# Optimization experiments

Measured on AMD Instinct MI355X. Metric: run time of the kernel, lower is better.

The kernel has to match this reference:

```python
import jax, jax.numpy as jnp
import numpy as np

N_NODES = 100000
N_EDGES = 3200000
DIN, DHID, DOUT = 128, 128, 128


def setup_inputs() -> dict:
    key = jax.random.key(0)
    ks = jax.random.split(key, 8)
    x = jax.random.normal(ks[0], (N_NODES, DIN), dtype=jnp.float32)
    edge_index = jax.random.randint(ks[1], (2, N_EDGES), 0, N_NODES, dtype=jnp.int32)
    def glorot(k, fan_in, fan_out):
        s = jnp.sqrt(6.0 / (fan_in + fan_out)).astype(jnp.float32)
        return jax.random.uniform(k, (fan_in, fan_out), jnp.float32, -s, s)
    return {
        "x": x,
        "edge_index": edge_index,
        "w1": glorot(ks[2], DIN, DHID), "b1": jnp.zeros((DHID,), jnp.float32),
        "w2": glorot(ks[3], DHID, DHID), "b2": jnp.zeros((DHID,), jnp.float32),
        "w3": glorot(ks[4], DHID, DOUT), "b3": jnp.zeros((DOUT,), jnp.float32),
    }


def reference(x, edge_index, w1, b1, w2, b2, w3, b3):
    n = x.shape[0]
    # GCN normalization with self-loops (PyG gcn_norm, edge_weight = 1)
    loop = jnp.arange(n, dtype=edge_index.dtype)
    src = jnp.concatenate([edge_index[0], loop])  # [E+N]
    dst = jnp.concatenate([edge_index[1], loop])  # [E+N]
    deg = jax.ops.segment_sum(jnp.ones_like(dst, dtype=x.dtype), dst, num_segments=n)
    dinv = jnp.where(deg > 0, jax.lax.rsqrt(deg), 0.0)
    norm = dinv[src] * dinv[dst]  # [E+N]

    def gcn_conv(h, w, b):
        h = h @ w  # [N, dout]
        msg = norm[:, None] * h[src]  # gather + scale, [E+N, dout]
        agg = jax.ops.segment_sum(msg, dst, num_segments=n)  # scatter-add
        return agg + b

    h = jax.nn.relu(gcn_conv(x, w1, b1))
    h = jax.nn.relu(gcn_conv(h, w2, b2))  # dropout p=0 / eval: no-op
    h = gcn_conv(h, w3, b3)
    return jnp.sum(h, axis=0, keepdims=True) / h.shape[0]  # [1, DOUT]
```

## Files before the change

### kernel.cpp

```cpp
#include <hip/hip_runtime.h>

#define D 128
#define BSH 8
#define CAP 12288
#define CH 8192

typedef unsigned short ushort_t;
typedef unsigned int uint_t;
typedef unsigned char uchar_t;

typedef __attribute__((ext_vector_type(8))) short frag_ab;
typedef __attribute__((ext_vector_type(4))) float frag_cd;
typedef __attribute__((ext_vector_type(2))) float float2v;

union frag_u { ushort_t u[8]; frag_ab v; };


__device__ __forceinline__ float bf2f(ushort_t u) {
    union { uint_t i; float f; } v; v.i = ((uint_t)u) << 16; return v.f;
}
__device__ __forceinline__ ushort_t f2bf(float f) {
    union { float f; uint_t i; } v; v.f = f;
    uint_t u = v.i;
    u += 0x7fffu + ((u >> 16) & 1u);
    return (ushort_t)(u >> 16);
}

__device__ __forceinline__ void acc_fp8(uint_t w, float2v& aA, float2v& aB) {
    aA += __builtin_amdgcn_cvt_pk_f32_fp8(w, false);
    aB += __builtin_amdgcn_cvt_pk_f32_fp8(w, true);
}
__device__ __forceinline__ uint_t g8(const uint_t* __restrict__ t8, uint_t byteoff) {
    return *(const uint_t*)((const char*)t8 + byteoff);
}

__launch_bounds__(512)
__global__ void k_binpack(const int* __restrict__ src, const int* __restrict__ dst,
                          int* __restrict__ curA, int* __restrict__ curB,
                          uint_t* __restrict__ binA, uint_t* __restrict__ binB,
                          int E, int nb, int nbin,
                          const float* __restrict__ W1, const float* __restrict__ W2,
                          ushort_t* __restrict__ h1, ushort_t* __restrict__ l1,
                          ushort_t* __restrict__ h2, ushort_t* __restrict__ l2,
                          const float* __restrict__ b1, const float* __restrict__ b2,
                          float* __restrict__ bp1, float* __restrict__ bp2,
                          uint_t* __restrict__ zrow) {
    int tx = threadIdx.x;

    if (blockIdx.x >= nbin) {
        int wb = blockIdx.x - nbin;
        if (wb == 64) {
            if (tx < 128) {
                int c = (tx & 7) * 16 + (tx >> 3);
                bp1[tx] = b1[c];
                bp2[tx] = b2[c];
            }
            if (tx >= 128 && tx < 160) zrow[tx - 128] = 0;
            return;
        }
        int gid = wb * 512 + tx;
        int which = gid >> 14;
        int idx = gid & 16383;
        int k = idx >> 7, n = idx & 127;
        float w = which ? W2[(((k & 7) * 16) + (k >> 3)) * 128 + n] : W1[idx];
        ushort_t h = f2bf(w);
        ushort_t l = f2bf(w - bf2f(h));
        int c = k >> 5, quad = (k >> 3) & 3, jj = k & 7;
        int j = n >> 4, l16 = n & 15;
        int lane = quad * 16 + l16;
        int dest = ((c * 8 + j) * 64 + lane) * 8 + jj;
        if (which) { h2[dest] = h; l2[dest] = l; }
        else       { h1[dest] = h; l1[dest] = l; }
        return;
    }

    __shared__ int hA[512], hB[512], sc[512], gb[512];
    __shared__ ushort_t sbkt[CH];
    __shared__ uint_t sent[CH];
    hA[tx] = 0; hB[tx] = 0;
    __syncthreads();

    int e0 = blockIdx.x * CH;
    int e1 = min(e0 + CH, E);
    int total = e1 - e0;

    int sreg[16], dreg[16];
#pragma unroll
    for (int it = 0; it < 16; ++it) {
        int e = e0 + tx + it * 512;
        if (e < e1) {
            int s = src[e], d = dst[e];
            sreg[it] = s; dreg[it] = d;
            atomicAdd(&hA[d >> BSH], 1);
            atomicAdd(&hB[s >> BSH], 1);
        }
    }
    __syncthreads();

    {
        int v = hA[tx];
        sc[tx] = v;
        __syncthreads();
        for (int d = 1; d < 512; d <<= 1) {
            int t = (tx >= d) ? sc[tx - d] : 0;
            __syncthreads();
            sc[tx] += t;
            __syncthreads();
        }
        sc[tx] -= v;
        gb[tx] = v ? atomicAdd(&curA[tx], v) : 0;
        hA[tx] = 0;
        __syncthreads();
#pragma unroll
        for (int it = 0; it < 16; ++it) {
            int e = e0 + tx + it * 512;
            if (e < e1) {
                int s = sreg[it], d = dreg[it];
                int k = d >> BSH;
                int pos = sc[k] + atomicAdd(&hA[k], 1);
                sent[pos] = ((uint_t)s << 8) | (uint_t)(d & 255);
                sbkt[pos] = (ushort_t)k;
            }
        }
        __syncthreads();
        for (int p = tx; p < total; p += 512) {
            int k = sbkt[p];
            int gp = gb[k] + (p - sc[k]);
            if (gp < CAP) binA[(size_t)k * CAP + gp] = sent[p];
        }
        __syncthreads();
    }

    {
        int v = hB[tx];
        sc[tx] = v;
        __syncthreads();
        for (int d = 1; d < 512; d <<= 1) {
            int t = (tx >= d) ? sc[tx - d] : 0;
            __syncthreads();
            sc[tx] += t;
            __syncthreads();
        }
        sc[tx] -= v;
        gb[tx] = v ? atomicAdd(&curB[tx], v) : 0;
        hB[tx] = 0;
        __syncthreads();
#pragma unroll
        for (int it = 0; it < 16; ++it) {
            int e = e0 + tx + it * 512;
            if (e < e1) {
                int s = sreg[it], d = dreg[it];
                int k = s >> BSH;
                int pos = sc[k] + atomicAdd(&hB[k], 1);
                sent[pos] = ((uint_t)d << 8) | (uint_t)(s & 255);
                sbkt[pos] = (ushort_t)k;
            }
        }
        __syncthreads();
        for (int p = tx; p < total; p += 512) {
            int k = sbkt[p];
            int gp = gb[k] + (p - sc[k]);
            if (gp < CAP) binB[(size_t)k * CAP + gp] = sent[p];
        }
    }
}

__launch_bounds__(1024)
__global__ void k_csr(const uint_t* __restrict__ binA, const int* __restrict__ curA,
                      float* __restrict__ dinv, int* __restrict__ row_beg,
                      int* __restrict__ row_end, int* __restrict__ csr_src, int N) {
    __shared__ int hist[256];
    __shared__ int scan[256];
    __shared__ uint_t ebuf[CAP];
    int b = blockIdx.x;
    int tx = threadIdx.x;
    int cnt = min(curA[b], CAP);
    const uint_t* eb = binA + (size_t)b * CAP;

    if (tx < 256) hist[tx] = 0;
    __syncthreads();
    for (int e = tx; e < cnt; e += 1024) {
        uint_t pk = eb[e];
        ebuf[e] = pk;
        atomicAdd(&hist[pk & 255u], 1);
    }
    __syncthreads();
    int v = 0, pd = 0;
    if (tx < 256) {
        v = hist[tx];
        pd = (v + 15) & ~15;
        scan[tx] = pd;
    }
    __syncthreads();
    for (int dd = 1; dd < 256; dd <<= 1) {
        int t = 0;
        if (tx < 256 && tx >= dd) t = scan[tx - dd];
        __syncthreads();
        if (tx < 256) scan[tx] += t;
        __syncthreads();
    }
    if (tx < 256) {
        int my_excl = scan[tx] - pd;
        int node = b * 256 + tx;
        if (node < N) {
            dinv[node] = rsqrtf((float)(v + 1));
            row_beg[node] = b * CAP + my_excl;
            row_end[node] = b * CAP + my_excl + pd;
        }
        for (int i = v; i < pd; i++)
            csr_src[b * CAP + my_excl + i] = N;
        hist[tx] = my_excl;
    }
    __syncthreads();
    for (int e = tx; e < cnt; e += 1024) {
        uint_t pk = ebuf[e];
        int pos = b * CAP + atomicAdd(&hist[pk & 255u], 1);
        csr_src[pos] = (int)(pk >> 8);
    }
}

template <int IN_F32>
__launch_bounds__(256)
__global__ void gemm_mfma(const void* __restrict__ Av, const ushort_t* __restrict__ Whi,
                          const ushort_t* __restrict__ Wlo, const float* __restrict__ dinv,
                          uchar_t* __restrict__ C8, int nrows) {
    int wave = threadIdx.x >> 6;
    int lane = threadIdx.x & 63;
    int quad = lane >> 4, l16 = lane & 15;
    int base = blockIdx.x * 128 + wave * 32;

    frag_cd acc[2][8];
#pragma unroll
    for (int rt = 0; rt < 2; rt++)
#pragma unroll
        for (int j = 0; j < 8; j++) acc[rt][j] = (frag_cd)0.f;

    const ushort_t* Ab = (const ushort_t*)Av;
    const float* Af = (const float*)Av;

#pragma unroll
    for (int c = 0; c < 4; c++) {
        frag_ab afrag[2];
        int koff = c * 32 + quad * 8;
#pragma unroll
        for (int rt = 0; rt < 2; rt++) {
            int row = min(base + rt * 16 + l16, nrows - 1);
            if (IN_F32) {
                const float* ap = Af + (size_t)row * D + koff;
                float4 a0 = *(const float4*)ap;
                float4 a1 = *(const float4*)(ap + 4);
                frag_u fu;
                fu.u[0] = f2bf(a0.x); fu.u[1] = f2bf(a0.y);
                fu.u[2] = f2bf(a0.z); fu.u[3] = f2bf(a0.w);
                fu.u[4] = f2bf(a1.x); fu.u[5] = f2bf(a1.y);
                fu.u[6] = f2bf(a1.z); fu.u[7] = f2bf(a1.w);
                afrag[rt] = fu.v;
            } else {
                afrag[rt] = *(const frag_ab*)(Ab + (size_t)row * D + koff);
            }
        }
#pragma unroll
        for (int j = 0; j < 8; j++) {
            frag_ab bh = *(const frag_ab*)(Whi + (((c * 8 + j) * 64 + lane) * 8));
            frag_ab bl = *(const frag_ab*)(Wlo + (((c * 8 + j) * 64 + lane) * 8));
#pragma unroll
            for (int rt = 0; rt < 2; rt++) {
                acc[rt][j] = __builtin_amdgcn_mfma_f32_16x16x32_bf16(afrag[rt], bh,
                                                                     acc[rt][j], 0, 0, 0);
                acc[rt][j] = __builtin_amdgcn_mfma_f32_16x16x32_bf16(afrag[rt], bl,
                                                                     acc[rt][j], 0, 0, 0);
            }
        }
    }

#pragma unroll
    for (int rt = 0; rt < 2; rt++) {
        int rbase = base + rt * 16 + quad * 4;
#pragma unroll
        for (int reg = 0; reg < 4; reg++) {
            int row = rbase + reg;
            if (row < nrows) {
                float dv = dinv[row];
                uint_t d0 = (uint_t)__builtin_amdgcn_cvt_pk_fp8_f32(
                    acc[rt][0][reg] * dv, acc[rt][1][reg] * dv, 0, false);
                d0 = (uint_t)__builtin_amdgcn_cvt_pk_fp8_f32(
                    acc[rt][2][reg] * dv, acc[rt][3][reg] * dv, (int)d0, true);
                uint_t d1 = (uint_t)__builtin_amdgcn_cvt_pk_fp8_f32(
                    acc[rt][4][reg] * dv, acc[rt][5][reg] * dv, 0, false);
                d1 = (uint_t)__builtin_amdgcn_cvt_pk_fp8_f32(
                    acc[rt][6][reg] * dv, acc[rt][7][reg] * dv, (int)d1, true);
                uint2 o; o.x = d0; o.y = d1;
                *(uint2*)(C8 + (size_t)row * D + l16 * 8) = o;
            }
        }
    }
}

__launch_bounds__(256)
__global__ void agg8(const uint_t* __restrict__ t8, const int* __restrict__ csr_src,
                     const int* __restrict__ row_beg, const int* __restrict__ row_end,
                     const float* __restrict__ dinv, const float* __restrict__ bias,
                     uint_t* __restrict__ out, int n, int do_relu) {
    int node = blockIdx.x * 4 + (threadIdx.x >> 6);
    if (node >= n) return;
    int lane = threadIdx.x & 63;
    int eh = lane >> 5;
    uint_t cl = (uint_t)(lane & 31);
    uint_t cl4 = cl * 4u;

    int beg = row_beg[node];
    int cnt = row_end[node] - beg;
    float dn = dinv[node];

    float2v accA = {0.f, 0.f}, accB = {0.f, 0.f};

    if (eh == 0) {
        uint_t w = g8(t8, (uint_t)node * 128u + cl4);
        accA = __builtin_amdgcn_cvt_pk_f32_fp8(w, false);
        accB = __builtin_amdgcn_cvt_pk_f32_fp8(w, true);
    }

    int half = cnt >> 1;
    int e     = beg + (eh ? half : 0);
    int nfull = half >> 3;

    uint4 sa, sb;
    if (nfull > 0) {
        __builtin_memcpy(&sa, csr_src + e, 16);
        __builtin_memcpy(&sb, csr_src + e + 4, 16);
    }
    for (int it = 0; it < nfull; ++it) {
        uint4 ca = sa, cb = sb;
        e += 8;
        if (it + 1 < nfull) {
            __builtin_memcpy(&sa, csr_src + e, 16);
            __builtin_memcpy(&sb, csr_src + e + 4, 16);
        }
        uint_t w0 = g8(t8, ca.x * 128u + cl4);
        uint_t w1 = g8(t8, ca.y * 128u + cl4);
        uint_t w2 = g8(t8, ca.z * 128u + cl4);
        uint_t w3 = g8(t8, ca.w * 128u + cl4);
        uint_t w4 = g8(t8, cb.x * 128u + cl4);
        uint_t w5 = g8(t8, cb.y * 128u + cl4);
        uint_t w6 = g8(t8, cb.z * 128u + cl4);
        uint_t w7 = g8(t8, cb.w * 128u + cl4);
        acc_fp8(w0, accA, accB);
        acc_fp8(w1, accA, accB);
        acc_fp8(w2, accA, accB);
        acc_fp8(w3, accA, accB);
        acc_fp8(w4, accA, accB);
        acc_fp8(w5, accA, accB);
        acc_fp8(w6, accA, accB);
        acc_fp8(w7, accA, accB);
    }

    float a0 = accA.x, a1 = accA.y, a2 = accB.x, a3 = accB.y;
    a0 += __shfl(a0, lane ^ 32, 64);
    a1 += __shfl(a1, lane ^ 32, 64);
    a2 += __shfl(a2, lane ^ 32, 64);
    a3 += __shfl(a3, lane ^ 32, 64);

    if (eh == 0) {
        float4 bb = ((const float4*)bias)[cl];
        float o0 = dn * a0 + bb.x;
        float o1 = dn * a1 + bb.y;
        float o2 = dn * a2 + bb.z;
        float o3 = dn * a3 + bb.w;
        if (do_relu) {
            o0 = fmaxf(o0, 0.f); o1 = fmaxf(o1, 0.f);
            o2 = fmaxf(o2, 0.f); o3 = fmaxf(o3, 0.f);
        }
        uint2 ow;
        ow.x = (uint_t)f2bf(o0) | ((uint_t)f2bf(o1) << 16);
        ow.y = (uint_t)f2bf(o2) | ((uint_t)f2bf(o3) << 16);
        ((uint2*)out)[(size_t)node * 32 + cl] = ow;
    }
}

__launch_bounds__(512)
__global__ void wreduce_fin(const ushort_t* __restrict__ h, const uint_t* __restrict__ binB,
                            const int* __restrict__ curB, const float* __restrict__ dinv,
                            float* __restrict__ v, int n,
                            const float* __restrict__ w3, const float* __restrict__ b3,
                            float* __restrict__ out, float invn, int* __restrict__ done) {
    __shared__ float owacc[256];
    __shared__ float s[512];
    __shared__ int is_last;
    int b = blockIdx.x;
    int tx = threadIdx.x;
    if (tx < 256) owacc[tx] = 0.f;
    __syncthreads();
    int cnt = min(curB[b], CAP);
    const uint_t* eb = binB + (size_t)b * CAP;
    for (int e = tx; e < cnt; e += 512) {
        uint_t pk = eb[e];
        atomicAdd(&owacc[pk & 255u], dinv[pk >> 8]);
    }
    __syncthreads();

    int c = tx & 127;
    int rg = tx >> 7;
    int base = b * 256;
    int lim = min(base + 256, n);
    float acc = 0.f;
    for (int r = base + rg; r < lim; r += 4) {
        float dv = dinv[r];
        float cv = dv * (dv + owacc[r - base]);
        acc += cv * bf2f(h[(size_t)r * D + c]);
    }
    s[tx] = acc;
    __syncthreads();
    if (tx < 128)
        atomicAdd(&v[c], (s[tx] + s[tx + 128]) + (s[tx + 256] + s[tx + 384]));
    __syncthreads();

    if (tx == 0) {
        __threadfence();
        int old = atomicAdd(done, 1);
        is_last = (old == (int)gridDim.x - 1) ? 1 : 0;
    }
    __syncthreads();
    if (is_last) {
        __threadfence();
        if (tx < 128) owacc[tx] = ((volatile float*)v)[tx];
        __syncthreads();
        if (tx < 128) {
            float facc = 0.f;
            for (int k = 0; k < D; k++) {
                int p = (k & 15) * 8 + (k >> 4);
                facc += owacc[p] * w3[(size_t)k * D + tx];
            }
            out[tx] = facc * invn + b3[tx];
        }
    }
}

extern "C" void kernel_launch(void* const* d_in, const int* in_sizes, int n_in,
                              void* d_out, int out_size, void* d_ws, size_t ws_size,
                              hipStream_t stream) {
    const float* x   = (const float*)d_in[0];
    const int*   ei  = (const int*)d_in[1];
    const float* w1  = (const float*)d_in[2];
    const float* b1  = (const float*)d_in[3];
    const float* w2  = (const float*)d_in[4];
    const float* b2  = (const float*)d_in[5];
    const float* w3  = (const float*)d_in[6];
    const float* b3  = (const float*)d_in[7];
    float* out = (float*)d_out;

    const int N = in_sizes[0] / D;
    const int E = in_sizes[1] / 2;
    const int* src = ei;
    const int* dst = ei + E;
    const int nb = (N + 255) >> 8;
    const int nbin = (E + CH - 1) / CH;

    char* p = (char*)d_ws;
    auto alloc = [&](size_t bytes) -> char* {
        char* r = p;
        p += (bytes + 255) & ~(size_t)255;
        return r;
    };
    char*     zbeg     = p;
    int*      curA     = (int*)alloc(512 * 4);
    int*      curB     = (int*)alloc(512 * 4);
    float*    v        = (float*)alloc((size_t)D * 4);
    int*      done     = (int*)alloc(256);
    char*     zend     = p;
    float*    dinv     = (float*)alloc((size_t)N * 4);
    int*      row_beg  = (int*)alloc((size_t)N * 4);
    int*      row_end  = (int*)alloc((size_t)N * 4);
    ushort_t* wp1h     = (ushort_t*)alloc(16384 * 2);
    ushort_t* wp1l     = (ushort_t*)alloc(16384 * 2);
    ushort_t* wp2h     = (ushort_t*)alloc(16384 * 2);
    ushort_t* wp2l     = (ushort_t*)alloc(16384 * 2);
    float*    bp1      = (float*)alloc(D * 4);
    float*    bp2      = (float*)alloc(D * 4);
    uint_t*   binA     = (uint_t*)alloc((size_t)nb * CAP * 4);
    uint_t*   binB     = (uint_t*)alloc((size_t)nb * CAP * 4);
    int*      csr_src  = (int*)alloc((size_t)nb * CAP * 4);
    ushort_t* bufH     = (ushort_t*)alloc((size_t)N * D * 2);
    uint_t*   buf8     = (uint_t*)alloc((size_t)(N + 1) * 32 * 4);
    (void)ws_size;

    const int gG = (N + 127) / 128;

    hipMemsetAsync(zbeg, 0, (size_t)(zend - zbeg), stream);

    k_binpack<<<nbin + 65, 512, 0, stream>>>(src, dst, curA, curB, binA, binB, E, nb,
                                             nbin, w1, w2, wp1h, wp1l, wp2h, wp2l,
                                             b1, b2, bp1, bp2, buf8 + (size_t)N * 32);
    k_csr<<<nb, 1024, 0, stream>>>(binA, curA, dinv, row_beg, row_end, csr_src, N);

    gemm_mfma<1><<<gG, 256, 0, stream>>>(x, wp1h, wp1l, dinv, (uchar_t*)buf8, N);
    agg8<<<(N + 3) / 4, 256, 0, stream>>>(buf8, csr_src, row_beg, row_end, dinv, bp1,
                                          (uint_t*)bufH, N, 1);
    gemm_mfma<0><<<gG, 256, 0, stream>>>(bufH, wp2h, wp2l, dinv, (uchar_t*)buf8, N);
    agg8<<<(N + 3) / 4, 256, 0, stream>>>(buf8, csr_src, row_beg, row_end, dinv, bp2,
                                          (uint_t*)bufH, N, 1);
    wreduce_fin<<<nb, 512, 0, stream>>>(bufH, binB, curB, dinv, v, N, w3, b3, out,
                                        1.0f / (float)N, done);
}
```

Baseline: 369.2 us.

## Move out-degree weight accumulation into first GEMM launch and split final reduction

The per-bin accumulation of source-side normalization weights is computed by extra blocks appended to the first GEMM launch, so it overlaps with matrix work instead of running serially in the final reduction kernel. The final reduction now uses smaller 128-row blocks that write per-block partial sums, and a separate single-block kernel sums them and applies W3, which replaces the global atomics and last-block detection. This adds one kernel launch and a partials buffer, but shortens the critical path of the tail kernel.

```diff
diff --git a/kernel.cpp b/kernel.cpp
--- a/kernel.cpp
+++ b/kernel.cpp
@@ -223,7 +223,26 @@
 __launch_bounds__(256)
 __global__ void gemm_mfma(const void* __restrict__ Av, const ushort_t* __restrict__ Whi,
                           const ushort_t* __restrict__ Wlo, const float* __restrict__ dinv,
-                          uchar_t* __restrict__ C8, int nrows) {
+                          uchar_t* __restrict__ C8, int nrows, int gemm_blocks,
+                          const uint_t* __restrict__ binB, const int* __restrict__ curB,
+                          float* __restrict__ ow) {
+    __shared__ float owacc[256];
+    if ((int)blockIdx.x >= gemm_blocks) {
+        int b = blockIdx.x - gemm_blocks;
+        int tx = threadIdx.x;
+        owacc[tx] = 0.f;
+        __syncthreads();
+        int cnt = min(curB[b], CAP);
+        const uint_t* eb = binB + (size_t)b * CAP;
+        for (int e = tx; e < cnt; e += 256) {
+            uint_t pk = eb[e];
+            atomicAdd(&owacc[pk & 255u], dinv[pk >> 8]);
+        }
+        __syncthreads();
+        ow[b * 256 + tx] = owacc[tx];
+        return;
+    }
+
     int wave = threadIdx.x >> 6;
     int lane = threadIdx.x & 63;
     int quad = lane >> 4, l16 = lane & 15;
@@ -378,60 +397,53 @@
 }
 
 __launch_bounds__(512)
-__global__ void wreduce_fin(const ushort_t* __restrict__ h, const uint_t* __restrict__ binB,
-                            const int* __restrict__ curB, const float* __restrict__ dinv,
-                            float* __restrict__ v, int n,
-                            const float* __restrict__ w3, const float* __restrict__ b3,
-                            float* __restrict__ out, float invn, int* __restrict__ done) {
-    __shared__ float owacc[256];
+__global__ void wreduce2(const ushort_t* __restrict__ h, const float* __restrict__ ow,
+                         const float* __restrict__ dinv, float* __restrict__ vpart,
+                         int n) {
     __shared__ float s[512];
-    __shared__ int is_last;
-    int b = blockIdx.x;
+    int bx = blockIdx.x;
     int tx = threadIdx.x;
-    if (tx < 256) owacc[tx] = 0.f;
-    __syncthreads();
-    int cnt = min(curB[b], CAP);
-    const uint_t* eb = binB + (size_t)b * CAP;
-    for (int e = tx; e < cnt; e += 512) {
-        uint_t pk = eb[e];
-        atomicAdd(&owacc[pk & 255u], dinv[pk >> 8]);
-    }
-    __syncthreads();
-
     int c = tx & 127;
     int rg = tx >> 7;
-    int base = b * 256;
-    int lim = min(base + 256, n);
+    int base = bx * 128;
+    int lim = min(base + 128, n);
     float acc = 0.f;
     for (int r = base + rg; r < lim; r += 4) {
         float dv = dinv[r];
-        float cv = dv * (dv + owacc[r - base]);
+        float cv = dv * (dv + ow[r]);
         acc += cv * bf2f(h[(size_t)r * D + c]);
     }
     s[tx] = acc;
     __syncthreads();
     if (tx < 128)
-        atomicAdd(&v[c], (s[tx] + s[tx + 128]) + (s[tx + 256] + s[tx + 384]));
-    __syncthreads();
-
-    if (tx == 0) {
-        __threadfence();
-        int old = atomicAdd(done, 1);
-        is_last = (old == (int)gridDim.x - 1) ? 1 : 0;
-    }
-    __syncthreads();
-    if (is_last) {
-        __threadfence();
-        if (tx < 128) owacc[tx] = ((volatile float*)v)[tx];
-        __syncthreads();
-        if (tx < 128) {
-            float facc = 0.f;
-            for (int k = 0; k < D; k++) {
-                int p = (k & 15) * 8 + (k >> 4);
-                facc += owacc[p] * w3[(size_t)k * D + tx];
-            }
-            out[tx] = facc * invn + b3[tx];
-        }
+        vpart[(size_t)bx * 128 + tx] =
+            (s[tx] + s[tx + 128]) + (s[tx + 256] + s[tx + 384]);
+}
+
+__launch_bounds__(512)
+__global__ void finalize2(const float* __restrict__ vpart, int nparts,
+                          const float* __restrict__ w3, const float* __restrict__ b3,
+                          float* __restrict__ out, float invn) {
+    __shared__ float s[512];
+    __shared__ float sv[D];
+    int tx = threadIdx.x;
+    int c = tx & 127;
+    int rg = tx >> 7;
+    float acc = 0.f;
+    for (int p = rg; p < nparts; p += 4)
+        acc += vpart[(size_t)p * 128 + c];
+    s[tx] = acc;
+    __syncthreads();
+    if (tx < 128)
+        sv[tx] = (s[tx] + s[tx + 128]) + (s[tx + 256] + s[tx + 384]);
+    __syncthreads();
+    if (tx < 128) {
+        float f2 = 0.f;
+        for (int k = 0; k < D; k++) {
+            int p = (k & 15) * 8 + (k >> 4);
+            f2 += sv[p] * w3[(size_t)k * D + tx];
+        }
+        out[tx] = f2 * invn + b3[tx];
     }
 }
 
@@ -454,6 +466,7 @@
     const int* dst = ei + E;
     const int nb = (N + 255) >> 8;
     const int nbin = (E + CH - 1) / CH;
+    const int nw2 = (N + 127) >> 7;
 
     char* p = (char*)d_ws;
     auto alloc = [&](size_t bytes) -> char* {
@@ -464,9 +477,9 @@
     char*     zbeg     = p;
     int*      curA     = (int*)alloc(512 * 4);
     int*      curB     = (int*)alloc(512 * 4);
-    float*    v        = (float*)alloc((size_t)D * 4);
-    int*      done     = (int*)alloc(256);
     char*     zend     = p;
+    float*    ow       = (float*)alloc((size_t)nb * 256 * 4);
+    float*    vpart    = (float*)alloc((size_t)nw2 * 128 * 4);
     float*    dinv     = (float*)alloc((size_t)N * 4);
     int*      row_beg  = (int*)alloc((size_t)N * 4);
     int*      row_end  = (int*)alloc((size_t)N * 4);
@@ -492,12 +505,14 @@
                                              b1, b2, bp1, bp2, buf8 + (size_t)N * 32);
     k_csr<<<nb, 1024, 0, stream>>>(binA, curA, dinv, row_beg, row_end, csr_src, N);
 
-    gemm_mfma<1><<<gG, 256, 0, stream>>>(x, wp1h, wp1l, dinv, (uchar_t*)buf8, N);
+    gemm_mfma<1><<<gG + nb, 256, 0, stream>>>(x, wp1h, wp1l, dinv, (uchar_t*)buf8, N,
+                                              gG, binB, curB, ow);
     agg8<<<(N + 3) / 4, 256, 0, stream>>>(buf8, csr_src, row_beg, row_end, dinv, bp1,
                                           (uint_t*)bufH, N, 1);
-    gemm_mfma<0><<<gG, 256, 0, stream>>>(bufH, wp2h, wp2l, dinv, (uchar_t*)buf8, N);
+    gemm_mfma<0><<<gG, 256, 0, stream>>>(bufH, wp2h, wp2l, dinv, (uchar_t*)buf8, N,
+                                         gG, binB, curB, ow);
     agg8<<<(N + 3) / 4, 256, 0, stream>>>(buf8, csr_src, row_beg, row_end, dinv, bp2,
                                           (uint_t*)bufH, N, 1);
-    wreduce_fin<<<nb, 512, 0, stream>>>(bufH, binB, curB, dinv, v, N, w3, b3, out,
-                                        1.0f / (float)N, done);
-}
+    wreduce2<<<nw2, 512, 0, stream>>>(bufH, ow, dinv, vpart, N);
+    finalize2<<<1, 512, 0, stream>>>(vpart, nw2, w3, b3, out, 1.0f / (float)N);
+}
```

New measurement: 396.5 us. 1.07x slower.
